# Optimization experiments

Hardware: AMD Instinct MI355X
Metric: run time of the kernel (lower is better)

Reference implementation:

```python
import jax, jax.numpy as jnp
import numpy as np

B, T, H, A, E, V = 32, 128, 1024, 1024, 512, 512  # A==H required by the module's cat/Linear shapes


def setup_inputs() -> dict:
    key = jax.random.key(0)
    ks = jax.random.split(key, 13)
    s = 0.02
    return {
        "encoder_outputs": jax.random.normal(ks[0], (B, A, E), jnp.float32),
        "hidden": jax.random.normal(ks[1], (1, B, H), jnp.float32),
        "target_seq": jax.random.normal(ks[2], (B, T, H), jnp.float32),
        "W_att": jax.random.normal(ks[3], (H + A, A), jnp.float32) * s,
        "b_att": jax.random.normal(ks[4], (A,), jnp.float32) * s,
        "W_comb": jax.random.normal(ks[5], (H + E, H), jnp.float32) * s,
        "b_comb": jax.random.normal(ks[6], (H,), jnp.float32) * s,
        "W_ih": jax.random.normal(ks[7], (3 * H, H), jnp.float32) * s,
        "b_ih": jax.random.normal(ks[8], (3 * H,), jnp.float32) * s,
        "W_hh": jax.random.normal(ks[9], (3 * H, H), jnp.float32) * s,
        "b_hh": jax.random.normal(ks[10], (3 * H,), jnp.float32) * s,
        "W_out": jax.random.normal(ks[11], (H, V), jnp.float32) * s,
        "b_out": jax.random.normal(ks[12], (V,), jnp.float32) * s,
    }


def reference(encoder_outputs, hidden, target_seq, W_att, b_att, W_comb, b_comb,
              W_ih, b_ih, W_hh, b_hh, W_out, b_out):
    # Teacher forcing: decoder input at step t is zeros (t=0) then target_seq[:, t-1]
    dec_in = jnp.concatenate([jnp.zeros_like(target_seq[:, :1]), target_seq[:, :-1]], axis=1)  # [B,T,H]
    dec_ts = jnp.swapaxes(dec_in, 0, 1)  # [T,B,H]

    def step(h, dec):  # h: [B,H], dec: [B,H]
        # attention over encoder positions (softmax width A == encoder seq len)
        attn = jax.nn.softmax(jnp.concatenate([dec, h], axis=1) @ W_att + b_att, axis=1)  # [B,A]
        ctx = jnp.einsum('bl,ble->be', attn, encoder_outputs)  # [B,E]
        g = jax.nn.relu(jnp.concatenate([dec, ctx], axis=1) @ W_comb + b_comb)  # [B,H]
        # GRU cell (torch gate order r, z, n)
        gi = g @ W_ih.T + b_ih
        gh = h @ W_hh.T + b_hh
        ir, iz, i_n = jnp.split(gi, 3, axis=1)
        hr, hz, h_n = jnp.split(gh, 3, axis=1)
        r = jax.nn.sigmoid(ir + hr)
        z = jax.nn.sigmoid(iz + hz)
        n = jnp.tanh(i_n + r * h_n)
        h_new = (1.0 - z) * n + z * h
        out_tok = h_new @ W_out + b_out  # [B,V]
        return h_new, out_tok

    h_last, outs = jax.lax.scan(step, hidden[0], dec_ts)  # outs: [T,B,V]
    output_seq = jnp.swapaxes(outs, 0, 1)  # [B,T,V]
    return output_seq, h_last[None]
```

## Files before the change

kernel.cpp:

```cpp
#include <hip/hip_runtime.h>

typedef unsigned short u16;
typedef unsigned int u32;
typedef unsigned long long u64;
typedef short v8s __attribute__((ext_vector_type(8)));
typedef float v4f __attribute__((ext_vector_type(4)));

#define MFMA16(a, b, c) __builtin_amdgcn_mfma_f32_16x16x32_bf16((a), (b), (c), 0, 0, 0)

#define B_ 32
#define T_ 128
#define H_ 1024
#define A_ 1024
#define E_ 512
#define V_ 512
#define NBLK 256
#define NTH 512
#define NSLOT 32
#define ENC_LDS_BYTES 131072
#define SCRATCH_BYTES 28672
#define DSMEM_BYTES (ENC_LDS_BYTES + SCRATCH_BYTES)

__device__ __forceinline__ float b2f(u16 u) {
  union { u32 u; float f; } c; c.u = ((u32)u) << 16; return c.f;
}
__device__ __forceinline__ u16 f2b(float f) {
  union { float f; u32 u; } c; c.f = f;
  u32 x = c.u;
  x += 0x7fffu + ((x >> 16) & 1u);
  return (u16)(x >> 16);
}

__device__ __forceinline__ void ato_st(u32* p, u32 v) {
  __hip_atomic_store(p, v, __ATOMIC_RELAXED, __HIP_MEMORY_SCOPE_AGENT);
}
__device__ __forceinline__ void ato_stf(float* p, float v) {
  union { float f; u32 u; } c; c.f = v; ato_st((u32*)p, c.u);
}
__device__ __forceinline__ void ato_addf(float* p, float v) {
  __hip_atomic_fetch_add(p, v, __ATOMIC_RELAXED, __HIP_MEMORY_SCOPE_AGENT);
}

__device__ __forceinline__ float ld4_sc1(const void* p) {
  float r;
  asm volatile("global_load_dword %0, %1, off sc1" : "=v"(r) : "v"(p));
  return r;
}
__device__ __forceinline__ void wait_vm0() {
  asm volatile("s_waitcnt vmcnt(0)" ::: "memory");
  __builtin_amdgcn_sched_barrier(0);
}
__device__ __forceinline__ void cvt8f(float4 qa, float4 qb, v8s& hi, v8s& lo) {
  float v[8] = {qa.x, qa.y, qa.z, qa.w, qb.x, qb.y, qb.z, qb.w};
  u16 hh[8], ll[8];
  #pragma unroll
  for (int i = 0; i < 8; ++i) {
    float x = fmaxf(v[i], 0.f);
    u16 hv = f2b(x);
    hh[i] = hv; ll[i] = f2b(x - b2f(hv));
  }
  hi = *(v8s*)hh; lo = *(v8s*)ll;
}

__device__ __forceinline__ void grid_bar(u32* arr, u32 ep) {
  asm volatile("s_waitcnt vmcnt(0)" ::: "memory");
  __syncthreads();
  if (threadIdx.x == 0)
    __hip_atomic_store(arr + blockIdx.x * NSLOT, ep, __ATOMIC_RELAXED, __HIP_MEMORY_SCOPE_AGENT);
  if (threadIdx.x < NBLK) {
    while (__hip_atomic_load(arr + threadIdx.x * NSLOT, __ATOMIC_RELAXED, __HIP_MEMORY_SCOPE_AGENT) < ep)
      __builtin_amdgcn_s_sleep(1);
  }
  __syncthreads();
  asm volatile("" ::: "memory");
}

__device__ __forceinline__ void gemm_nk(const u16* ah, const u16* al, size_t mstr,
                                        const u16* bp, int nk, v4f& c0, v4f& c1) {
  #pragma unroll 2
  for (int i = 0; i < nk; ++i) {
    v8s b   = *(const v8s*)(bp);
    v8s a0h = *(const v8s*)(ah);
    v8s a1h = *(const v8s*)(ah + mstr);
    v8s a0l = *(const v8s*)(al);
    v8s a1l = *(const v8s*)(al + mstr);
    c0 = MFMA16(a0h, b, c0);
    c1 = MFMA16(a1h, b, c1);
    c0 = MFMA16(a0l, b, c0);
    c1 = MFMA16(a1l, b, c1);
    ah += 32; al += 32; bp += 32;
  }
}

__device__ __forceinline__ void red_store2(float* part, int wv, int lane, v4f c0, v4f c1) {
  float* p = part + (wv * 64 + lane) * 8;
  #pragma unroll
  for (int r = 0; r < 4; ++r) { p[r] = c0[r]; p[4 + r] = c1[r]; }
}
__device__ __forceinline__ float red_sum2(const float* part, int o) {
  int m = o >> 4, n = o & 15;
  int lane = (((m & 15) >> 2) << 4) + n;
  int idx = ((m >> 4) << 2) + (m & 3);
  float s = 0.f;
  #pragma unroll
  for (int w = 0; w < 8; ++w) s += part[(w * 64 + lane) * 8 + idx];
  return s;
}

__global__ void __launch_bounds__(NTH, 1)
dec_persist(const u16* __restrict__ WattT, const u16* __restrict__ Whh_b,
            const u16* __restrict__ Wih_b, const u16* __restrict__ Wc_ctxT,
            const float* __restrict__ enc_f,
            const float* __restrict__ bih, const float* __restrict__ bhh,
            const float* __restrict__ ldec_all,
            float* h, float* logit, float* gh, float* g_all,
            u16* hs_hi, u16* hs_lo, u32* bar)
{
  const int tid = threadIdx.x;
  const int bid = blockIdx.x;
  const int lane = tid & 63;
  const int wv = tid >> 6;
  const int ln = lane & 15;
  const int kq8 = (lane >> 4) * 8;

  extern __shared__ __align__(16) unsigned char dsm[];
  u16* lds_enc = (u16*)dsm;
  float* scratch = (float*)(dsm + ENC_LDS_BYTES);

  {
    int b = bid >> 3, e0 = (bid & 7) * 64;
    const float* src = enc_f + (size_t)b * A_ * E_ + e0 + (tid & 7) * 8;
    int seg = (tid & 7) * 8;
    for (int i = 0; i < 16; ++i) {
      int row = i * 64 + (tid >> 3);
      const float* sp = src + (size_t)row * E_;
      float4 a = *(const float4*)sp;
      float4 bq = *(const float4*)(sp + 4);
      u16 tmp[8] = {f2b(a.x), f2b(a.y), f2b(a.z), f2b(a.w),
                    f2b(bq.x), f2b(bq.y), f2b(bq.z), f2b(bq.w)};
      *(v8s*)(lds_enc + row * 64 + seg) = *(v8s*)tmp;
    }
  }

  u32 ep = 0;

  for (int t = 0; t < T_; ++t) {
    {
      float* part = scratch;
      const u16* hb = hs_hi + (size_t)t * (B_ * H_);
      const u16* lb = hs_lo + (size_t)t * (B_ * H_);
      size_t a0 = (size_t)ln * H_ + wv * 128 + kq8;
      v8s ah0[4], ah1[4], al0[4], al1[4];
      #pragma unroll
      for (int i = 0; i < 4; ++i) {
        ah0[i] = *(const v8s*)(hb + a0 + i * 32);
        ah1[i] = *(const v8s*)(hb + a0 + 16 * H_ + i * 32);
        al0[i] = *(const v8s*)(lb + a0 + i * 32);
        al1[i] = *(const v8s*)(lb + a0 + 16 * H_ + i * 32);
      }
      float ldec = 0.f;
      const u16* bp;
      int n0;
      if (bid < 64) {
        n0 = bid * 16;
        ldec = ldec_all[(size_t)t * (B_ * A_) + (tid >> 4) * A_ + n0 + (tid & 15)];
        bp = WattT + (size_t)(n0 + ln) * 2048 + 1024 + wv * 128 + kq8;
      } else {
        n0 = (bid - 64) * 16;
        bp = Whh_b + (size_t)(n0 + ln) * H_ + wv * 128 + kq8;
      }
      v4f c0 = {0.f, 0.f, 0.f, 0.f}, c1 = {0.f, 0.f, 0.f, 0.f};
      #pragma unroll
      for (int i = 0; i < 4; ++i) {
        v8s wb = *(const v8s*)(bp + i * 32);
        c0 = MFMA16(ah0[i], wb, c0);
        c1 = MFMA16(ah1[i], wb, c1);
        c0 = MFMA16(al0[i], wb, c0);
        c1 = MFMA16(al1[i], wb, c1);
      }
      red_store2(part, wv, lane, c0, c1);
      __syncthreads();
      {
        float s = red_sum2(part, tid);
        int m = tid >> 4, n = tid & 15;
        if (bid < 64) {
          ato_stf(&logit[m * A_ + n0 + n], s + ldec);
        } else {
          ato_stf(&gh[(size_t)(n0 + n) * 32 + m], s + bhh[n0 + n]);
        }
      }
    }
    grid_bar(bar, ++ep);

    {
      float* p    = scratch;
      float* part = scratch + 1024;
      float* red  = scratch + 5120;
      float* sctx = scratch + 5136;
      int b = bid >> 3, es = bid & 7;
      float v1 = ld4_sc1(&logit[b * A_ + tid]);
      float v2 = ld4_sc1(&logit[b * A_ + 512 + tid]);
      wait_vm0();
      float mx = fmaxf(v1, v2);
      #pragma unroll
      for (int off = 32; off; off >>= 1) mx = fmaxf(mx, __shfl_xor(mx, off));
      if (lane == 0) red[wv] = mx;
      __syncthreads();
      float mfull = red[0];
      #pragma unroll
      for (int q = 1; q < 8; ++q) mfull = fmaxf(mfull, red[q]);
      float e1 = __expf(v1 - mfull), e2 = __expf(v2 - mfull);
      p[tid] = e1; p[512 + tid] = e2;
      float sm = e1 + e2;
      #pragma unroll
      for (int off = 32; off; off >>= 1) sm += __shfl_xor(sm, off);
      if (lane == 0) red[8 + wv] = sm;
      __syncthreads();
      float ssum = red[8];
      #pragma unroll
      for (int q = 1; q < 8; ++q) ssum += red[8 + q];
      float inv = 1.f / ssum;

      int le = lane & 7, lr = lane >> 3;
      float acc[8] = {0.f, 0.f, 0.f, 0.f, 0.f, 0.f, 0.f, 0.f};
      #pragma unroll 4
      for (int i = 0; i < 16; ++i) {
        int l = i * 64 + wv * 8 + lr;
        v8s w = *(const v8s*)(lds_enc + l * 64 + le * 8);
        float pv = p[l];
        #pragma unroll
        for (int r = 0; r < 8; ++r) acc[r] += pv * b2f((u16)w[r]);
      }
      float* pp = part + ((wv * 8 + lr) * 8 + le) * 8;
      #pragma unroll
      for (int r = 0; r < 8; ++r) pp[r] = acc[r];
      __syncthreads();
      if (tid < 64) {
        int eo = tid >> 3, r = tid & 7;
        float s = 0.f;
        #pragma unroll
        for (int q = 0; q < 64; ++q) s += part[q * 64 + eo * 8 + r];
        sctx[tid] = s * inv;
      }
      __syncthreads();
      {
        const u16* w0 = Wc_ctxT + (size_t)(2 * tid) * E_ + es * 64;
        const u16* w1 = w0 + E_;
        float a0 = 0.f, a1 = 0.f;
        #pragma unroll
        for (int i = 0; i < 8; ++i) {
          v8s q0 = *(const v8s*)(w0 + i * 8);
          v8s q1 = *(const v8s*)(w1 + i * 8);
          #pragma unroll
          for (int r = 0; r < 8; ++r) {
            float pv = sctx[i * 8 + r];
            a0 += pv * b2f((u16)q0[r]);
            a1 += pv * b2f((u16)q1[r]);
          }
        }
        float* gp = g_all + (size_t)t * (B_ * H_) + b * H_ + 2 * tid;
        ato_addf(gp, a0);
        ato_addf(gp + 1, a1);
      }
    }
    grid_bar(bar, ++ep);

    {
      if (bid < 64) {
        float* part = scratch;
        float* hx   = scratch + 6144;
        int j0 = bid * 16;
        const float* gbase = g_all + (size_t)t * (B_ * H_);
        int koff0 = wv * 128 + kq8;
        float4 ga[4][2], gb[4][2];
        #pragma unroll
        for (int i = 0; i < 4; ++i) {
          const float* p0 = gbase + (size_t)ln * H_ + koff0 + i * 32;
          const float* p1 = gbase + (size_t)(ln + 16) * H_ + koff0 + i * 32;
          ga[i][0] = *(const float4*)p0; ga[i][1] = *(const float4*)(p0 + 4);
          gb[i][0] = *(const float4*)p1; gb[i][1] = *(const float4*)(p1 + 4);
        }
        const u16* bp0 = Wih_b + (size_t)(j0 + ln) * H_ + koff0;
        const u16* bp1 = bp0 + (size_t)H_ * H_;
        const u16* bp2 = bp0 + (size_t)2 * H_ * H_;
        v4f c00 = {0.f,0.f,0.f,0.f}, c01 = c00, c02 = c00, c10 = c00, c11 = c00, c12 = c00;
        #pragma unroll
        for (int i = 0; i < 4; ++i) {
          v8s wb0 = *(const v8s*)(bp0 + i * 32);
          v8s wb1 = *(const v8s*)(bp1 + i * 32);
          v8s wb2 = *(const v8s*)(bp2 + i * 32);
          v8s a0h, a0l, a1h, a1l;
          cvt8f(ga[i][0], ga[i][1], a0h, a0l);
          cvt8f(gb[i][0], gb[i][1], a1h, a1l);
          c00 = MFMA16(a0h, wb0, c00); c00 = MFMA16(a0l, wb0, c00);
          c01 = MFMA16(a0h, wb1, c01); c01 = MFMA16(a0l, wb1, c01);
          c02 = MFMA16(a0h, wb2, c02); c02 = MFMA16(a0l, wb2, c02);
          c10 = MFMA16(a1h, wb0, c10); c10 = MFMA16(a1l, wb0, c10);
          c11 = MFMA16(a1h, wb1, c11); c11 = MFMA16(a1l, wb1, c11);
          c12 = MFMA16(a1h, wb2, c12); c12 = MFMA16(a1l, wb2, c12);
        }
        float hr0 = 0.f, hz0 = 0.f, hn0 = 0.f, hr1 = 0.f, hz1 = 0.f, hn1 = 0.f;
        float ho0 = 0.f, ho1 = 0.f;
        int obl = tid >> 4, jj = tid & 15, j = j0 + jj;
        if (tid < 256) {
          hr0 = ld4_sc1(&gh[(size_t)j * 32 + obl]);
          hz0 = ld4_sc1(&gh[(size_t)(H_ + j) * 32 + obl]);
          hn0 = ld4_sc1(&gh[(size_t)(2 * H_ + j) * 32 + obl]);
          hr1 = ld4_sc1(&gh[(size_t)j * 32 + 16 + obl]);
          hz1 = ld4_sc1(&gh[(size_t)(H_ + j) * 32 + 16 + obl]);
          hn1 = ld4_sc1(&gh[(size_t)(2 * H_ + j) * 32 + 16 + obl]);
          ho0 = h[obl * H_ + j];
          ho1 = h[(obl + 16) * H_ + j];
        }
        float bi_r = 0.f, bi_z = 0.f, bi_n = 0.f;
        if (tid < 256) {
          bi_r = bih[j]; bi_z = bih[H_ + j]; bi_n = bih[2 * H_ + j];
        }
        #pragma unroll
        for (int pass = 0; pass < 2; ++pass) {
          float* pp = part + (wv * 64 + lane) * 12;
          if (pass == 0) {
            #pragma unroll
            for (int r = 0; r < 4; ++r) { pp[r] = c00[r]; pp[4 + r] = c01[r]; pp[8 + r] = c02[r]; }
          } else {
            #pragma unroll
            for (int r = 0; r < 4; ++r) { pp[r] = c10[r]; pp[4 + r] = c11[r]; pp[8 + r] = c12[r]; }
          }
          __syncthreads();
          if (tid < 256) {
            if (pass == 0) wait_vm0();
            int ob = pass * 16 + obl;
            int lanei = ((obl >> 2) << 4) + jj;
            int rg = obl & 3;
            float ir = 0.f, iz = 0.f, in_ = 0.f;
            #pragma unroll
            for (int w = 0; w < 8; ++w) {
              const float* q = part + (w * 64 + lanei) * 12;
              ir += q[rg]; iz += q[4 + rg]; in_ += q[8 + rg];
            }
            ir += bi_r; iz += bi_z; in_ += bi_n;
            float hr = pass ? hr1 : hr0;
            float hz = pass ? hz1 : hz0;
            float hn = pass ? hn1 : hn0;
            float ho = pass ? ho1 : ho0;
            float r = 1.f / (1.f + __expf(-(ir + hr)));
            float z = 1.f / (1.f + __expf(-(iz + hz)));
            float n = tanhf(in_ + r * hn);
            float hnew = (1.f - z) * n + z * ho;
            h[ob * H_ + j] = hnew;
            hx[ob * 16 + jj] = hnew;
          }
          __syncthreads();
        }
        if (tid < 256) {
          int ob2 = tid >> 3, j2 = (tid & 7) * 2;
          float v0 = hx[ob2 * 16 + j2], v1 = hx[ob2 * 16 + j2 + 1];
          u16 h0 = f2b(v0), h1 = f2b(v1);
          u16 l0 = f2b(v0 - b2f(h0)), l1 = f2b(v1 - b2f(h1));
          size_t idx = (size_t)(t + 1) * (B_ * H_) + ob2 * H_ + j0 + j2;
          ato_st((u32*)(hs_hi + idx), (u32)h0 | ((u32)h1 << 16));
          ato_st((u32*)(hs_lo + idx), (u32)l0 | ((u32)l1 << 16));
        }
      }
    }
    grid_bar(bar, ++ep);
  }
}

__global__ void __launch_bounds__(256)
dec_gemm(const u16* __restrict__ th, const u16* __restrict__ tl,
         const u16* __restrict__ W, const unsigned long wstride,
         const float* __restrict__ bias, float* __restrict__ out)
{
  int tid = threadIdx.x, lane = tid & 63, wv = tid >> 6;
  int ln = lane & 15, kq8 = (lane >> 4) * 8;
  int t = blockIdx.x >> 4, nt = blockIdx.x & 15;
  float* op = out + (size_t)t * (32 * 1024);
  if (t == 0) {
    for (int i = tid; i < 32 * 64; i += 256) {
      int b = i >> 6, n = nt * 64 + (i & 63);
      ato_stf(&op[(size_t)b * 1024 + n], bias[n]);
    }
    return;
  }
  int n0w = nt * 64 + wv * 16;
  const u16* ah = th + ((size_t)ln * T_ + (t - 1)) * H_ + kq8;
  const u16* al = tl + ((size_t)ln * T_ + (t - 1)) * H_ + kq8;
  const u16* bp = W + (size_t)(n0w + ln) * wstride + kq8;
  v4f c0 = {0.f, 0.f, 0.f, 0.f}, c1 = {0.f, 0.f, 0.f, 0.f};
  gemm_nk(ah, al, (size_t)16 * T_ * H_, bp, 32, c0, c1);
  int n = n0w + (lane & 15);
  float bo = bias[n];
  int rb = (lane >> 4) * 4;
  #pragma unroll
  for (int r = 0; r < 4; ++r) {
    ato_stf(&op[(size_t)(rb + r) * 1024 + n], c0[r] + bo);
    ato_stf(&op[(size_t)(rb + r + 16) * 1024 + n], c1[r] + bo);
  }
}

__global__ void __launch_bounds__(256, 2)
out_gemm(const u16* __restrict__ hseq, const u16* __restrict__ WoutT,
         const float* __restrict__ bout, float* __restrict__ out)
{
  int tid = threadIdx.x, lane = tid & 63, wv = tid >> 6;
  int ln = lane & 15, kq8 = (lane >> 4) * 8;
  int m0 = (blockIdx.x >> 3) * 32;
  int n0 = (blockIdx.x & 7) * 64 + wv * 16;
  v4f c0 = {0.f, 0.f, 0.f, 0.f}, c1 = {0.f, 0.f, 0.f, 0.f};
  const u16* ap = hseq + (size_t)(m0 + ln) * 1024 + kq8;
  const u16* bp = WoutT + (size_t)(n0 + ln) * 1024 + kq8;
  for (int i = 0; i < 32; ++i) {
    v8s b = *(const v8s*)bp;
    v8s a0 = *(const v8s*)ap;
    v8s a1 = *(const v8s*)(ap + 16 * 1024);
    c0 = MFMA16(a0, b, c0);
    c1 = MFMA16(a1, b, c1);
    ap += 32; bp += 32;
  }
  int v = n0 + ln;
  float bo = bout[v];
  int rbase = (lane >> 4) * 4;
  #pragma unroll
  for (int rg = 0; rg < 4; ++rg) {
    int m = m0 + rbase + rg;
    out[((size_t)(m & 31) * T_ + (m >> 5)) * V_ + v] = c0[rg] + bo;
    int m2 = m + 16;
    out[((size_t)(m2 & 31) * T_ + (m2 >> 5)) * V_ + v] = c1[rg] + bo;
  }
}

__global__ void __launch_bounds__(256)
hlast_copy(const float* __restrict__ h, float* __restrict__ out)
{
  int i = blockIdx.x * 256 + threadIdx.x;
  if (i < B_ * H_) out[(size_t)B_ * T_ * V_ + i] = h[i];
}

__global__ void __launch_bounds__(256)
k_cvt(const float* __restrict__ in, u16* __restrict__ out, int n)
{
  int stride = gridDim.x * 256;
  for (int i = blockIdx.x * 256 + threadIdx.x; i < n; i += stride) out[i] = f2b(in[i]);
}

__global__ void __launch_bounds__(256)
k_cvt_split(const float* __restrict__ in, u16* __restrict__ hi, u16* __restrict__ lo, int n)
{
  int stride = gridDim.x * 256;
  for (int i = blockIdx.x * 256 + threadIdx.x; i < n; i += stride) {
    float x = in[i];
    u16 a = f2b(x);
    hi[i] = a;
    lo[i] = f2b(x - b2f(a));
  }
}

__global__ void __launch_bounds__(256)
k_tr(const float* __restrict__ in, u16* __restrict__ out, int R, int C)
{
  __shared__ float tile[32][33];
  int tc = C >> 5;
  int r0 = (blockIdx.x / tc) << 5, c0 = (blockIdx.x % tc) << 5;
  int tx = threadIdx.x & 31, ty = threadIdx.x >> 5;
  #pragma unroll
  for (int q = 0; q < 4; ++q) {
    int r = ty + q * 8;
    tile[r][tx] = in[(size_t)(r0 + r) * C + c0 + tx];
  }
  __syncthreads();
  #pragma unroll
  for (int q = 0; q < 4; ++q) {
    int r = ty + q * 8;
    out[(size_t)(c0 + r) * R + r0 + tx] = f2b(tile[tx][r]);
  }
}

__global__ void __launch_bounds__(256)
k_init(const float* __restrict__ hidden, float* h, u16* hs_hi, u16* hs_lo)
{
  int i = blockIdx.x * 256 + threadIdx.x;
  if (i < B_ * H_) {
    float x = hidden[i];
    h[i] = x;
    u16 a = f2b(x);
    hs_hi[i] = a;
    hs_lo[i] = f2b(x - b2f(a));
  }
}

extern "C" void kernel_launch(void* const* d_in, const int* in_sizes, int n_in,
                              void* d_out, int out_size, void* d_ws, size_t ws_size,
                              hipStream_t stream) {
  (void)in_sizes; (void)n_in; (void)out_size; (void)ws_size;
  const float* enc    = (const float*)d_in[0];
  const float* hidden = (const float*)d_in[1];
  const float* tgt    = (const float*)d_in[2];
  const float* Watt   = (const float*)d_in[3];
  const float* batt   = (const float*)d_in[4];
  const float* Wcomb  = (const float*)d_in[5];
  const float* bcomb  = (const float*)d_in[6];
  const float* Wih    = (const float*)d_in[7];
  const float* bih    = (const float*)d_in[8];
  const float* Whh    = (const float*)d_in[9];
  const float* bhh    = (const float*)d_in[10];
  const float* Wout   = (const float*)d_in[11];
  const float* bout   = (const float*)d_in[12];

  size_t off = 0;
  char* base = (char*)d_ws;
  auto alloc = [&](size_t bytes) -> void* {
    void* p = base + off;
    off += (bytes + 255) & ~(size_t)255;
    return p;
  };
  size_t bar_bytes = (size_t)(NBLK * NSLOT + 64) * 4;
  u32*   bar    = (u32*)  alloc(bar_bytes);
  float* h      = (float*)alloc(B_ * H_ * 4);
  float* logit  = (float*)alloc(B_ * A_ * 4);
  float* gh     = (float*)alloc((size_t)3 * H_ * B_ * 4);
  float* ldec_all = (float*)alloc((size_t)T_ * B_ * A_ * 4);
  float* g_all    = (float*)alloc((size_t)T_ * B_ * H_ * 4);
  u16*   hs_hi  = (u16*)  alloc((size_t)(T_ + 1) * B_ * H_ * 2);
  u16*   hs_lo  = (u16*)  alloc((size_t)(T_ + 1) * B_ * H_ * 2);
  u16*   tgt_hi = (u16*)  alloc((size_t)B_ * T_ * H_ * 2);
  u16*   tgt_lo = (u16*)  alloc((size_t)B_ * T_ * H_ * 2);
  u16*   WattT  = (u16*)  alloc((size_t)2048 * 1024 * 2);
  u16*   Whh_b  = (u16*)  alloc((size_t)3 * H_ * H_ * 2);
  u16*   Wih_b  = (u16*)  alloc((size_t)3 * H_ * H_ * 2);
  u16*   WcombT = (u16*)  alloc((size_t)1024 * 1536 * 2);
  u16*   Wc_ctxT= (u16*)  alloc((size_t)1024 * 512 * 2);
  u16*   WoutT  = (u16*)  alloc((size_t)512 * 1024 * 2);

  hipMemsetAsync(bar, 0, bar_bytes, stream);

  k_cvt_split<<<2048, 256, 0, stream>>>(tgt, tgt_hi, tgt_lo, B_ * T_ * H_);
  k_cvt<<<2048, 256, 0, stream>>>(Whh, Whh_b, 3 * H_ * H_);
  k_cvt<<<2048, 256, 0, stream>>>(Wih, Wih_b, 3 * H_ * H_);
  k_tr<<<64 * 32, 256, 0, stream>>>(Watt, WattT, 2048, 1024);
  k_tr<<<48 * 32, 256, 0, stream>>>(Wcomb, WcombT, 1536, 1024);
  k_tr<<<16 * 32, 256, 0, stream>>>(Wcomb + (size_t)1024 * H_, Wc_ctxT, 512, 1024);
  k_tr<<<32 * 16, 256, 0, stream>>>(Wout, WoutT, 1024, 512);
  k_init<<<128, 256, 0, stream>>>(hidden, h, hs_hi, hs_lo);

  dec_gemm<<<2048, 256, 0, stream>>>(tgt_hi, tgt_lo, WattT, 2048UL, batt, ldec_all);
  dec_gemm<<<2048, 256, 0, stream>>>(tgt_hi, tgt_lo, WcombT, 1536UL, bcomb, g_all);

  hipFuncSetAttribute((const void*)dec_persist,
                      hipFuncAttributeMaxDynamicSharedMemorySize, DSMEM_BYTES);

  dec_persist<<<NBLK, NTH, DSMEM_BYTES, stream>>>(WattT, Whh_b, Wih_b, Wc_ctxT, enc,
                                                  bih, bhh, ldec_all,
                                                  h, logit, gh, g_all,
                                                  hs_hi, hs_lo, bar);
  out_gemm<<<1024, 256, 0, stream>>>(hs_hi + B_ * H_, WoutT, bout, (float*)d_out);
  hlast_copy<<<128, 256, 0, stream>>>(h, (float*)d_out);
}
```

Before: 4.164 ms.

## Compact barrier slots, halve phase-1 blocks with wider tiles, batch loads before MFMAs

The grid barrier now uses contiguous per-block slots instead of one slot per cache line, and waits with a longer sleep. Phase 1 (attention logits and W_hh gates) now runs on 128 blocks, each computing two 16-column tiles, instead of 256 blocks with one tile each. It also loads activations through sc1 cache-bypass loads. Phase 1 and the W_ih phase now issue all activation and weight loads before a single wait, so memory latency overlaps before the MFMA chain. The aim is to cut barrier polling cost and per-step load latency, at the price of less parallelism in phase 1, extra reductions and possible contention on the packed barrier slots.

```diff
diff --git a/kernel.cpp b/kernel.cpp
--- a/kernel.cpp
+++ b/kernel.cpp
@@ -5,6 +5,7 @@
 typedef unsigned long long u64;
 typedef short v8s __attribute__((ext_vector_type(8)));
 typedef float v4f __attribute__((ext_vector_type(4)));
+typedef int v4i __attribute__((ext_vector_type(4)));
 
 #define MFMA16(a, b, c) __builtin_amdgcn_mfma_f32_16x16x32_bf16((a), (b), (c), 0, 0, 0)
 
@@ -16,7 +17,6 @@
 #define V_ 512
 #define NBLK 256
 #define NTH 512
-#define NSLOT 32
 #define ENC_LDS_BYTES 131072
 #define SCRATCH_BYTES 28672
 #define DSMEM_BYTES (ENC_LDS_BYTES + SCRATCH_BYTES)
@@ -41,6 +41,11 @@
   __hip_atomic_fetch_add(p, v, __ATOMIC_RELAXED, __HIP_MEMORY_SCOPE_AGENT);
 }
 
+__device__ __forceinline__ v4i ld16_sc1(const void* p) {
+  v4i r;
+  asm volatile("global_load_dwordx4 %0, %1, off sc1" : "=v"(r) : "v"(p));
+  return r;
+}
 __device__ __forceinline__ float ld4_sc1(const void* p) {
   float r;
   asm volatile("global_load_dword %0, %1, off sc1" : "=v"(r) : "v"(p));
@@ -50,8 +55,11 @@
   asm volatile("s_waitcnt vmcnt(0)" ::: "memory");
   __builtin_amdgcn_sched_barrier(0);
 }
-__device__ __forceinline__ void cvt8f(float4 qa, float4 qb, v8s& hi, v8s& lo) {
-  float v[8] = {qa.x, qa.y, qa.z, qa.w, qb.x, qb.y, qb.z, qb.w};
+__device__ __forceinline__ v8s as8(v4i x) { union { v4i a; v8s b; } u; u.a = x; return u.b; }
+__device__ __forceinline__ void cvt8(v4i qa, v4i qb, v8s& hi, v8s& lo) {
+  union { v4i q; float f[4]; } a, b;
+  a.q = qa; b.q = qb;
+  float v[8] = {a.f[0], a.f[1], a.f[2], a.f[3], b.f[0], b.f[1], b.f[2], b.f[3]};
   u16 hh[8], ll[8];
   #pragma unroll
   for (int i = 0; i < 8; ++i) {
@@ -62,14 +70,14 @@
   hi = *(v8s*)hh; lo = *(v8s*)ll;
 }
 
-__device__ __forceinline__ void grid_bar(u32* arr, u32 ep) {
+__device__ __forceinline__ void grid_bar(u32* slots, u32 ep) {
   asm volatile("s_waitcnt vmcnt(0)" ::: "memory");
   __syncthreads();
   if (threadIdx.x == 0)
-    __hip_atomic_store(arr + blockIdx.x * NSLOT, ep, __ATOMIC_RELAXED, __HIP_MEMORY_SCOPE_AGENT);
+    __hip_atomic_store(slots + blockIdx.x, ep, __ATOMIC_RELAXED, __HIP_MEMORY_SCOPE_AGENT);
   if (threadIdx.x < NBLK) {
-    while (__hip_atomic_load(arr + threadIdx.x * NSLOT, __ATOMIC_RELAXED, __HIP_MEMORY_SCOPE_AGENT) < ep)
-      __builtin_amdgcn_s_sleep(1);
+    while (__hip_atomic_load(slots + threadIdx.x, __ATOMIC_RELAXED, __HIP_MEMORY_SCOPE_AGENT) < ep)
+      __builtin_amdgcn_s_sleep(2);
   }
   __syncthreads();
   asm volatile("" ::: "memory");
@@ -145,49 +153,69 @@
   u32 ep = 0;
 
   for (int t = 0; t < T_; ++t) {
-    {
+    if (bid < 128) {
       float* part = scratch;
       const u16* hb = hs_hi + (size_t)t * (B_ * H_);
       const u16* lb = hs_lo + (size_t)t * (B_ * H_);
       size_t a0 = (size_t)ln * H_ + wv * 128 + kq8;
-      v8s ah0[4], ah1[4], al0[4], al1[4];
+      v4i ah0[4], ah1[4], al0[4], al1[4];
       #pragma unroll
       for (int i = 0; i < 4; ++i) {
-        ah0[i] = *(const v8s*)(hb + a0 + i * 32);
-        ah1[i] = *(const v8s*)(hb + a0 + 16 * H_ + i * 32);
-        al0[i] = *(const v8s*)(lb + a0 + i * 32);
-        al1[i] = *(const v8s*)(lb + a0 + 16 * H_ + i * 32);
-      }
-      float ldec = 0.f;
-      const u16* bp;
+        ah0[i] = ld16_sc1(hb + a0 + i * 32);
+        ah1[i] = ld16_sc1(hb + a0 + 16 * H_ + i * 32);
+        al0[i] = ld16_sc1(lb + a0 + i * 32);
+        al1[i] = ld16_sc1(lb + a0 + 16 * H_ + i * 32);
+      }
+      const u16* bpA;
+      size_t bstride;
+      float ldec0 = 0.f, ldec1 = 0.f;
       int n0;
-      if (bid < 64) {
-        n0 = bid * 16;
-        ldec = ldec_all[(size_t)t * (B_ * A_) + (tid >> 4) * A_ + n0 + (tid & 15)];
-        bp = WattT + (size_t)(n0 + ln) * 2048 + 1024 + wv * 128 + kq8;
+      if (bid < 32) {
+        n0 = bid * 32;
+        const float* lp = ldec_all + (size_t)t * (B_ * A_) + (tid >> 4) * A_ + n0 + (tid & 15);
+        ldec0 = lp[0];
+        ldec1 = lp[16];
+        bpA = WattT + (size_t)(n0 + ln) * 2048 + 1024 + wv * 128 + kq8;
+        bstride = 2048;
       } else {
-        n0 = (bid - 64) * 16;
-        bp = Whh_b + (size_t)(n0 + ln) * H_ + wv * 128 + kq8;
-      }
-      v4f c0 = {0.f, 0.f, 0.f, 0.f}, c1 = {0.f, 0.f, 0.f, 0.f};
+        n0 = (bid - 32) * 32;
+        bpA = Whh_b + (size_t)(n0 + ln) * H_ + wv * 128 + kq8;
+        bstride = H_;
+      }
+      const u16* bpB = bpA + 16 * bstride;
+      v8s wA[4], wB[4];
       #pragma unroll
       for (int i = 0; i < 4; ++i) {
-        v8s wb = *(const v8s*)(bp + i * 32);
-        c0 = MFMA16(ah0[i], wb, c0);
-        c1 = MFMA16(ah1[i], wb, c1);
-        c0 = MFMA16(al0[i], wb, c0);
-        c1 = MFMA16(al1[i], wb, c1);
-      }
-      red_store2(part, wv, lane, c0, c1);
+        wA[i] = *(const v8s*)(bpA + i * 32);
+        wB[i] = *(const v8s*)(bpB + i * 32);
+      }
+      v4f cA0 = {0.f,0.f,0.f,0.f}, cA1 = cA0, cB0 = cA0, cB1 = cA0;
+      wait_vm0();
+      #pragma unroll
+      for (int i = 0; i < 4; ++i) {
+        v8s h0 = as8(ah0[i]), h1 = as8(ah1[i]);
+        v8s l0 = as8(al0[i]), l1 = as8(al1[i]);
+        cA0 = MFMA16(h0, wA[i], cA0); cA1 = MFMA16(h1, wA[i], cA1);
+        cA0 = MFMA16(l0, wA[i], cA0); cA1 = MFMA16(l1, wA[i], cA1);
+        cB0 = MFMA16(h0, wB[i], cB0); cB1 = MFMA16(h1, wB[i], cB1);
+        cB0 = MFMA16(l0, wB[i], cB0); cB1 = MFMA16(l1, wB[i], cB1);
+      }
+      red_store2(part, wv, lane, cA0, cA1);
       __syncthreads();
       {
         float s = red_sum2(part, tid);
         int m = tid >> 4, n = tid & 15;
-        if (bid < 64) {
-          ato_stf(&logit[m * A_ + n0 + n], s + ldec);
-        } else {
-          ato_stf(&gh[(size_t)(n0 + n) * 32 + m], s + bhh[n0 + n]);
-        }
+        if (bid < 32) ato_stf(&logit[m * A_ + n0 + n], s + ldec0);
+        else          ato_stf(&gh[(size_t)(n0 + n) * 32 + m], s + bhh[n0 + n]);
+      }
+      __syncthreads();
+      red_store2(part, wv, lane, cB0, cB1);
+      __syncthreads();
+      {
+        float s = red_sum2(part, tid);
+        int m = tid >> 4, n = tid & 15;
+        if (bid < 32) ato_stf(&logit[m * A_ + n0 + 16 + n], s + ldec1);
+        else          ato_stf(&gh[(size_t)(n0 + 16 + n) * 32 + m], s + bhh[n0 + 16 + n]);
       }
     }
     grid_bar(bar, ++ep);
@@ -272,32 +300,39 @@
         int j0 = bid * 16;
         const float* gbase = g_all + (size_t)t * (B_ * H_);
         int koff0 = wv * 128 + kq8;
-        float4 ga[4][2], gb[4][2];
+        v4i gr0[8], gr1[8];
         #pragma unroll
         for (int i = 0; i < 4; ++i) {
           const float* p0 = gbase + (size_t)ln * H_ + koff0 + i * 32;
           const float* p1 = gbase + (size_t)(ln + 16) * H_ + koff0 + i * 32;
-          ga[i][0] = *(const float4*)p0; ga[i][1] = *(const float4*)(p0 + 4);
-          gb[i][0] = *(const float4*)p1; gb[i][1] = *(const float4*)(p1 + 4);
+          gr0[2 * i]     = ld16_sc1(p0);
+          gr0[2 * i + 1] = ld16_sc1(p0 + 4);
+          gr1[2 * i]     = ld16_sc1(p1);
+          gr1[2 * i + 1] = ld16_sc1(p1 + 4);
         }
         const u16* bp0 = Wih_b + (size_t)(j0 + ln) * H_ + koff0;
         const u16* bp1 = bp0 + (size_t)H_ * H_;
         const u16* bp2 = bp0 + (size_t)2 * H_ * H_;
+        v8s wb0[4], wb1[4], wb2[4];
+        #pragma unroll
+        for (int i = 0; i < 4; ++i) {
+          wb0[i] = *(const v8s*)(bp0 + i * 32);
+          wb1[i] = *(const v8s*)(bp1 + i * 32);
+          wb2[i] = *(const v8s*)(bp2 + i * 32);
+        }
         v4f c00 = {0.f,0.f,0.f,0.f}, c01 = c00, c02 = c00, c10 = c00, c11 = c00, c12 = c00;
+        wait_vm0();
         #pragma unroll
         for (int i = 0; i < 4; ++i) {
-          v8s wb0 = *(const v8s*)(bp0 + i * 32);
-          v8s wb1 = *(const v8s*)(bp1 + i * 32);
-          v8s wb2 = *(const v8s*)(bp2 + i * 32);
           v8s a0h, a0l, a1h, a1l;
-          cvt8f(ga[i][0], ga[i][1], a0h, a0l);
-          cvt8f(gb[i][0], gb[i][1], a1h, a1l);
-          c00 = MFMA16(a0h, wb0, c00); c00 = MFMA16(a0l, wb0, c00);
-          c01 = MFMA16(a0h, wb1, c01); c01 = MFMA16(a0l, wb1, c01);
-          c02 = MFMA16(a0h, wb2, c02); c02 = MFMA16(a0l, wb2, c02);
-          c10 = MFMA16(a1h, wb0, c10); c10 = MFMA16(a1l, wb0, c10);
-          c11 = MFMA16(a1h, wb1, c11); c11 = MFMA16(a1l, wb1, c11);
-          c12 = MFMA16(a1h, wb2, c12); c12 = MFMA16(a1l, wb2, c12);
+          cvt8(gr0[2 * i], gr0[2 * i + 1], a0h, a0l);
+          cvt8(gr1[2 * i], gr1[2 * i + 1], a1h, a1l);
+          c00 = MFMA16(a0h, wb0[i], c00); c00 = MFMA16(a0l, wb0[i], c00);
+          c01 = MFMA16(a0h, wb1[i], c01); c01 = MFMA16(a0l, wb1[i], c01);
+          c02 = MFMA16(a0h, wb2[i], c02); c02 = MFMA16(a0l, wb2[i], c02);
+          c10 = MFMA16(a1h, wb0[i], c10); c10 = MFMA16(a1l, wb0[i], c10);
+          c11 = MFMA16(a1h, wb1[i], c11); c11 = MFMA16(a1l, wb1[i], c11);
+          c12 = MFMA16(a1h, wb2[i], c12); c12 = MFMA16(a1l, wb2[i], c12);
         }
         float hr0 = 0.f, hz0 = 0.f, hn0 = 0.f, hr1 = 0.f, hz1 = 0.f, hn1 = 0.f;
         float ho0 = 0.f, ho1 = 0.f;
@@ -514,8 +549,7 @@
     off += (bytes + 255) & ~(size_t)255;
     return p;
   };
-  size_t bar_bytes = (size_t)(NBLK * NSLOT + 64) * 4;
-  u32*   bar    = (u32*)  alloc(bar_bytes);
+  u32*   bar    = (u32*)  alloc(1024);
   float* h      = (float*)alloc(B_ * H_ * 4);
   float* logit  = (float*)alloc(B_ * A_ * 4);
   float* gh     = (float*)alloc((size_t)3 * H_ * B_ * 4);
@@ -532,7 +566,7 @@
   u16*   Wc_ctxT= (u16*)  alloc((size_t)1024 * 512 * 2);
   u16*   WoutT  = (u16*)  alloc((size_t)512 * 1024 * 2);
 
-  hipMemsetAsync(bar, 0, bar_bytes, stream);
+  hipMemsetAsync(bar, 0, 1024, stream);
 
   k_cvt_split<<<2048, 256, 0, stream>>>(tgt, tgt_hi, tgt_lo, B_ * T_ * H_);
   k_cvt<<<2048, 256, 0, stream>>>(Whh, Whh_b, 3 * H_ * H_);
```

Result: slower. 5.850 ms (+40.5%).
